# Optimization experiments

Hardware: AMD Instinct MI355X
Metric: run time of the kernel (lower is better)

The kernel has to match this reference:

```python
import jax, jax.numpy as jnp
import numpy as np

R, S, M, K = 512, 48, 4096, 16
RADIUS = 4.0 * 0.025
DIMS = [511, 256, 256, 256, 3]


def posenc(x, n_freqs):
    freqs = 2.0 ** jnp.arange(n_freqs, dtype=x.dtype)
    xf = x[..., None, :] * freqs[:, None]            # [..., F, C]
    sc = jnp.stack([jnp.sin(xf), jnp.cos(xf)], -2)   # [..., F, 2, C]
    return jnp.concatenate([x, sc.reshape(x.shape[:-1] + (-1,))], -1)


def ball_query(q, p, radius, k):
    # pytorch3d-style: first k points (by index order) within radius.
    # dists are squared distances, 0 for padding; neighbors are 0 for padding; idx -1 for padding.
    d2 = jnp.sum((q[:, None, :] - p[None, :, :]) ** 2, -1)    # [Nq, M]
    m = p.shape[0]
    order = jnp.where(d2 < radius * radius, jnp.arange(m), m)
    neg, idx = jax.lax.top_k(-order, k)                        # k smallest valid indices
    valid = neg > -m
    dists = jnp.where(valid, jnp.take_along_axis(d2, idx, axis=1), 0.0)
    nbrs = jnp.where(valid[..., None], p[idx], 0.0)
    return dists, jnp.where(valid, idx, -1), nbrs


def setup_inputs() -> dict:
    key = jax.random.key(0)
    ks = jax.random.split(key, 16)
    inp = {
        "points": jax.random.uniform(ks[0], (R, S, 3), jnp.float32),
        "normals": jax.random.normal(ks[1], (R * S, 3), jnp.float32),
        "view_dirs": jax.random.normal(ks[2], (R * S, 3), jnp.float32),
        "feature_vectors": jax.random.normal(ks[3], (R * S, 256), jnp.float32),
        "indices": 0,
        "physical_particles": jax.random.uniform(ks[4], (M, 3), jnp.float32),
        "rays": jax.random.normal(ks[5], (R, 6), jnp.float32),
        "ro": jax.random.normal(ks[6], (1, 3), jnp.float32),
    }
    for l in range(4):
        scale = (2.0 / DIMS[l + 1]) ** 0.5
        inp[f"W{l}"] = jax.random.normal(ks[7 + l], (DIMS[l + 1], DIMS[l]), jnp.float32) * scale
        inp[f"b{l}"] = jnp.zeros((DIMS[l + 1],), jnp.float32)
    return inp


def reference(points, normals, view_dirs, feature_vectors, indices, physical_particles,
              rays, ro, W0, b0, W1, b1, W2, b2, W3, b3):
    q = points.reshape(-1, 3)                                     # [R*S, 3]
    dists, idx, nbrs = ball_query(q, physical_particles, RADIUS, K)
    dists = dists.reshape(R, S, K)
    nbrs = nbrs.reshape(R, S, K, 3)
    nn_mask = dists != 0                                          # padded entries have dist 0
    num_nn = nn_mask.sum(-1, keepdims=True)                       # [R, S, 1]

    hit_pos_emb = posenc(q, 10)                                   # [R*S, 63]
    hit_dir_emb = jnp.repeat(posenc(rays[:, 3:], 4), S, axis=0)   # [R*S, 27]

    # smoothing_position (exclude_ray=True)
    dn = jnp.linalg.norm(nbrs - points[:, :, None, :], axis=-1)   # [R, S, K]
    w = jnp.maximum(1.0 - (dn / RADIUS) ** 3, 0.0)
    density = w.sum(-1, keepdims=True)                            # [R, S, 1]
    smoothed = (w[..., None] * nbrs).sum(-2) / (density + 1e-12)  # [R, S, 3]

    sp = smoothed.reshape(-1, 3)
    dirs = sp - ro
    dirs = dirs / jnp.linalg.norm(dirs, axis=-1, keepdims=True)

    density_emb = posenc(density.reshape(-1, 1), 4)               # [R*S, 9]
    smoothed_pos_emb = posenc(sp, 10)                             # [R*S, 63]

    # masked variance of neighbor offsets
    diff = jnp.where(nn_mask[..., None], nbrs - points[:, :, None, :], 0.0)
    mean = diff.sum(-2) / (num_nn + 1e-12)
    var = jnp.where(nn_mask[..., None], (diff - mean[:, :, None, :]) ** 2, 0.0).sum(-2) / (num_nn + 1e-12)
    var_emb = posenc(var.reshape(-1, 3), 10)                      # [R*S, 63]

    x = jnp.concatenate([hit_pos_emb, density_emb, smoothed_pos_emb, var_emb,
                         hit_dir_emb, posenc(dirs, 4), normals, feature_vectors], -1)  # [R*S, 511]

    for Wl, bl in ((W0, b0), (W1, b1), (W2, b2)):
        x = jax.nn.relu(x @ Wl.T + bl)
    return jax.nn.sigmoid(x @ W3.T + b3)
```

## Files before the change

### kernel.cpp

```cpp
#include <hip/hip_runtime.h>

typedef _Float16 f16;
typedef f16 f16x8 __attribute__((ext_vector_type(8)));
typedef float f32x4 __attribute__((ext_vector_type(4)));
typedef unsigned short u16;

__device__ __forceinline__ void glds16(const void* g, void* l) {
  __builtin_amdgcn_global_load_lds(
      (const __attribute__((address_space(1))) unsigned*)g,
      (__attribute__((address_space(3))) unsigned*)l, 16, 0, 0);
}


struct FT {
  u16 v[256];
  static constexpr u16 enc(int s, int f, int k) {
    return (u16)(s | (f << 5) | (k << 9));
  }
  constexpr void p3(int base, int F, int src) {
    v[base + 0] = enc(src + 0, 0, 0);
    v[base + 1] = enc(src + 1, 0, 0);
    v[base + 2] = enc(src + 2, 0, 0);
    for (int f = 0; f < F; ++f)
      for (int r = 0; r < 6; ++r) {
        int comp = (r < 3) ? r : r - 3;
        v[base + 3 + f * 6 + r] = enc(src + comp, f, (r < 3) ? 1 : 2);
      }
  }
  constexpr void p1(int base, int F, int src) {
    v[base] = enc(src, 0, 0);
    for (int f = 0; f < F; ++f) {
      v[base + 1 + 2 * f] = enc(src, f, 1);
      v[base + 2 + 2 * f] = enc(src, f, 2);
    }
  }
  constexpr FT() : v{} {
    p3(0, 10, 0);
    p1(63, 4, 3);
    p3(72, 10, 4);
    p3(135, 10, 7);
    p3(198, 4, 10);
    p3(225, 4, 13);
    v[252] = enc(16, 0, 0);
    v[253] = enc(17, 0, 0);
    v[254] = enc(18, 0, 0);
    v[255] = enc(0, 0, 3);
  }
};
__constant__ FT ftab = FT();

__device__ float4 g_sorted[4096];
__device__ int    g_cellStart[1001];

__global__ __launch_bounds__(1024) void setup_kernel(
    const float* __restrict__ parts,
    const float* __restrict__ W0, const float* __restrict__ W1,
    const float* __restrict__ W2,
    f16* __restrict__ w0f, f16* __restrict__ w1f, f16* __restrict__ w2f)
{
  const int tid = threadIdx.x;
  if (blockIdx.x < 256) {
    int i = blockIdx.x * 1024 + tid;
    float v; f16* pf; int n, c;
    if (i < 131072) {
      n = i >> 9; c = i & 511;
      v = (c < 255) ? W0[n * 511 + c] : ((c == 255) ? 0.0f : W0[n * 511 + (c - 1)]);
      pf = w0f;
    } else if (i < 196608) {
      int j = i - 131072; n = j >> 8; c = j & 255; v = W1[j]; pf = w1f;
    } else {
      int j = i - 196608; n = j >> 8; c = j & 255; v = W2[j]; pf = w2f;
    }
    int kt = c >> 5, g = (c >> 3) & 3, jj = c & 7;
    int u = n * 4 + (g ^ ((n >> 1) & 3));
    pf[kt * 8192 + u * 8 + jj] = (f16)v;
  } else {
    __shared__ int cnt[1000];
    __shared__ int pos[1000];
    __shared__ int wpre[125];
    for (int j = tid; j < 1000; j += 1024) cnt[j] = 0;
    __syncthreads();

    float px[4], py[4], pz[4];
    int cd[4];
    #pragma unroll
    for (int t = 0; t < 4; ++t) {
      int i = tid + t * 1024;
      float x = parts[3 * i], y = parts[3 * i + 1], z = parts[3 * i + 2];
      int cx = min(max((int)(x * 10.0f), 0), 9);
      int cy = min(max((int)(y * 10.0f), 0), 9);
      int cz = min(max((int)(z * 10.0f), 0), 9);
      cd[t] = (cz * 10 + cy) * 10 + cx;
      px[t] = x; py[t] = y; pz[t] = z;
      atomicAdd(&cnt[cd[t]], 1);
    }
    __syncthreads();

    if (tid < 125) {
      int s = 0;
      #pragma unroll
      for (int k = 0; k < 8; ++k) s += cnt[tid * 8 + k];
      wpre[tid] = s;
    }
    __syncthreads();
    if (tid == 0) {
      int s = 0;
      for (int c = 0; c < 125; ++c) { int t = wpre[c]; wpre[c] = s; s += t; }
    }
    __syncthreads();
    if (tid < 125) {
      int run = wpre[tid];
      #pragma unroll
      for (int k = 0; k < 8; ++k) {
        int c = tid * 8 + k;
        int n = cnt[c];
        pos[c] = run;
        g_cellStart[c] = run;
        run += n;
      }
    }
    if (tid == 0) g_cellStart[1000] = 4096;
    __syncthreads();

    #pragma unroll
    for (int t = 0; t < 4; ++t) {
      int p = atomicAdd(&pos[cd[t]], 1);
      g_sorted[p] = make_float4(px[t], py[t], pz[t], __int_as_float(tid + t * 1024));
    }
  }
}

#define MAXCH 5

__global__ __launch_bounds__(256) void feat_kernel(
    const float* __restrict__ points, const float* __restrict__ normals,
    const float* __restrict__ parts, const float* __restrict__ rays,
    const float* __restrict__ ro, f16* __restrict__ Xf)
{
  __shared__ float sdata[4][20];

  const int tid = threadIdx.x;
  const int lane = tid & 63, wv = tid >> 6;
  const int q = blockIdx.x * 4 + wv;
  const float qx = points[3 * q], qy = points[3 * q + 1], qz = points[3 * q + 2];
  const float RQ = 0.1f * 0.1f;

  int nAcc = 0;
  float sdx = 0, sdy = 0, sdz = 0;
  float s2x = 0, s2y = 0, s2z = 0;
  float sw = 0, swx = 0, swy = 0, swz = 0;

  const int cqx = min(max((int)(qx * 10.0f), 0), 9);
  const int cqy = min(max((int)(qy * 10.0f), 0), 9);
  const int cqz = min(max((int)(qz * 10.0f), 0), 9);

  int st_l = 0, cn_l = 0;
  if (lane < 9) {
    int dz = lane / 3, dy = lane - dz * 3;
    int cz = cqz - 1 + dz, cy = cqy - 1 + dy;
    if ((unsigned)cz <= 9u && (unsigned)cy <= 9u) {
      int x0 = max(cqx - 1, 0), x1 = min(cqx + 1, 9);
      int rb = (cz * 10 + cy) * 10;
      st_l = g_cellStart[rb + x0];
      cn_l = g_cellStart[rb + x1 + 1] - st_l;
    }
  }

  int pk[9], bk[9];
  int run = 0;
  #pragma unroll
  for (int k = 0; k < 9; ++k) {
    int stk = __builtin_amdgcn_readlane(st_l, k);
    int cnk = __builtin_amdgcn_readlane(cn_l, k);
    pk[k] = run;
    bk[k] = stk - run;
    run += cnk;
  }
  const int C = run;
  const bool fb = (C > MAXCH * 64);

  if (!fb) {
    float4 sv[MAXCH];
    int iv[MAXCH];
    unsigned long long hm[MAXCH];
    #pragma unroll
    for (int ch = 0; ch < MAXCH; ++ch) {
      if (ch * 64 < C) {
        int s = ch * 64 + lane;
        int g = bk[0];
        #pragma unroll
        for (int k = 1; k < 9; ++k) g = (s >= pk[k]) ? bk[k] : g;
        float4 pt = g_sorted[min(g + s, 4095)];
        if (s >= C) {
          pt.x = 1e9f; pt.y = 1e9f; pt.z = 1e9f;
          pt.w = __int_as_float(0x7fffffff);
        }
        sv[ch] = pt;
        iv[ch] = __float_as_int(pt.w);
        float ex = pt.x - qx, ey = pt.y - qy, ez = pt.z - qz;
        float d2 = __fadd_rn(__fadd_rn(__fmul_rn(ex, ex), __fmul_rn(ey, ey)),
                             __fmul_rn(ez, ez));
        hm[ch] = __ballot(d2 < RQ);
      } else {
        hm[ch] = 0ULL;
      }
    }

    int N = 0;
    #pragma unroll
    for (int ch = 0; ch < MAXCH; ++ch) N += __popcll(hm[ch]);

    int thr = 0x7fffffff;
    if (N > 16) {
      int lo = 0, hi = 4095;
      while (lo < hi) {
        int mid = (lo + hi) >> 1;
        int c = 0;
        #pragma unroll
        for (int ch = 0; ch < MAXCH; ++ch)
          if (ch * 64 < C)
            c += __popcll(hm[ch] & __ballot(iv[ch] <= mid));
        if (c >= 16) hi = mid; else lo = mid + 1;
      }
      thr = lo;
    }

    #pragma unroll
    for (int ch = 0; ch < MAXCH; ++ch) {
      if (ch * 64 < C) {
        float4 pt = sv[ch];
        float ex = pt.x - qx, ey = pt.y - qy, ez = pt.z - qz;
        float d2 = __fadd_rn(__fadd_rn(__fmul_rn(ex, ex), __fmul_rn(ey, ey)),
                             __fmul_rn(ez, ez));
        if (d2 < RQ && iv[ch] <= thr) {
          nAcc++;
          sdx += ex; sdy += ey; sdz += ez;
          s2x += ex * ex; s2y += ey * ey; s2z += ez * ez;
          float dn = sqrtf(d2);
          float t = dn * 10.0f;
          float w = fmaxf(1.0f - t * t * t, 0.0f);
          sw += w; swx += w * pt.x; swy += w * pt.y; swz += w * pt.z;
        }
      }
    }
  } else {
    int total = 0;
    for (int jr = 0; jr < 64; ++jr) {
      int pi = jr * 64 + lane;
      float x = parts[3 * pi], y = parts[3 * pi + 1], z = parts[3 * pi + 2];
      float ex = x - qx, ey = y - qy, ez = z - qz;
      float d2 = __fadd_rn(__fadd_rn(__fmul_rn(ex, ex), __fmul_rn(ey, ey)),
                           __fmul_rn(ez, ez));
      bool hit = d2 < RQ;
      unsigned long long m = __ballot(hit);
      int pos = __builtin_amdgcn_mbcnt_hi((unsigned)(m >> 32),
                __builtin_amdgcn_mbcnt_lo((unsigned)m, 0u));
      if (hit && (total + pos < 16)) {
        nAcc++;
        sdx += ex; sdy += ey; sdz += ez;
        s2x += ex * ex; s2y += ey * ey; s2z += ez * ez;
        float dn = sqrtf(d2);
        float t = dn * 10.0f;
        float w = fmaxf(1.0f - t * t * t, 0.0f);
        sw += w; swx += w * x; swy += w * y; swz += w * z;
      }
      total += __popcll(m);
      if (total >= 16) break;
    }
  }

  #define WRED(x) { _Pragma("unroll") for (int o = 32; o; o >>= 1) x += __shfl_xor(x, o, 64); }
  float fn = (float)nAcc;
  WRED(fn); WRED(sdx); WRED(sdy); WRED(sdz);
  WRED(s2x); WRED(s2y); WRED(s2z);
  WRED(sw); WRED(swx); WRED(swy); WRED(swz);
  #undef WRED

  float tq = sqrtf(qx * qx + qy * qy + qz * qz) * 10.0f;
  float wpad = fmaxf(1.0f - tq * tq * tq, 0.0f);
  float density = sw + (16.0f - fn) * wpad;
  float invd = 1.0f / (density + 1e-12f);
  float spx = swx * invd, spy = swy * invd, spz = swz * invd;

  float invn = 1.0f / (fn + 1e-12f);
  float mx = sdx * invn, my = sdy * invn, mz = sdz * invn;
  float vx = fmaxf((s2x - 2.0f * mx * sdx + fn * mx * mx) * invn, 0.0f);
  float vy = fmaxf((s2y - 2.0f * my * sdy + fn * my * my) * invn, 0.0f);
  float vz = fmaxf((s2z - 2.0f * mz * sdz + fn * mz * mz) * invn, 0.0f);

  float dxx = spx - ro[0], dyy = spy - ro[1], dzz = spz - ro[2];
  float il = 1.0f / sqrtf(dxx * dxx + dyy * dyy + dzz * dzz);

  if (lane == 0) {
    float* s = sdata[wv];
    s[0] = qx; s[1] = qy; s[2] = qz; s[3] = density;
    s[4] = spx; s[5] = spy; s[6] = spz;
    s[7] = vx; s[8] = vy; s[9] = vz;
    int r = q / 48;
    s[10] = rays[6 * r + 3]; s[11] = rays[6 * r + 4]; s[12] = rays[6 * r + 5];
    s[13] = dxx * il; s[14] = dyy * il; s[15] = dzz * il;
    s[16] = normals[3 * q]; s[17] = normals[3 * q + 1]; s[18] = normals[3 * q + 2];
  }
  __syncthreads();

  const int b = q / 48, m48 = q % 48;
  const size_t base = (size_t)b * 12288;
  #pragma unroll
  for (int it = 0; it < 4; ++it) {
    int c = it * 64 + lane;
    int e = ftab.v[c];
    float sv_ = sdata[wv][e & 31];
    float arg = sv_ * (float)(1 << ((e >> 5) & 15));
    float sn, cs;
    __sincosf(arg, &sn, &cs);
    int kind = e >> 9;
    float val = (kind == 0) ? sv_ : (kind == 1 ? sn : (kind == 2 ? cs : 0.0f));
    int kt = c >> 5, g = (c >> 3) & 3, j = c & 7;
    int u = m48 * 4 + (g ^ ((m48 >> 1) & 3));
    Xf[base + kt * 1536 + u * 8 + j] = (f16)val;
  }
}

__global__ __launch_bounds__(512, 6) void fused_mlp(
    const f16* __restrict__ Xf, const float* __restrict__ fvec,
    const f16* __restrict__ w0f, const f16* __restrict__ w1f,
    const f16* __restrict__ w2f,
    const float* __restrict__ b0, const float* __restrict__ b1,
    const float* __restrict__ b2,
    const float* __restrict__ W3, const float* __restrict__ b3,
    float* __restrict__ out)
{
  extern __shared__ char lds[];
  f16* As = (f16*)lds;
  f16* Hf = (f16*)lds;
  f16* H2 = (f16*)(lds + 24576);
  float* w3s = (float*)(lds + 49152);

  const int tid = threadIdx.x, lane = tid & 63, wn = tid >> 6;
  const int l15 = lane & 15, l4 = lane >> 4;
  const int blk = blockIdx.x;

  f32x4 acc[3][2];
  f16x8 bq[4][2];
  f16x8 af[2][3];

  const f16* Xft = Xf + (size_t)blk * 12288;

  int uB[2];
  #pragma unroll
  for (int j = 0; j < 2; ++j) {
    int n = wn * 32 + j * 16 + l15;
    uB[j] = n * 4 + (l4 ^ ((n >> 1) & 3));
  }
  int uA[3];
  #pragma unroll
  for (int i = 0; i < 3; ++i) {
    int m = i * 16 + l15;
    uA[i] = m * 4 + (l4 ^ ((m >> 1) & 3));
  }

  auto zacc = [&]() {
    #pragma unroll
    for (int i = 0; i < 3; ++i)
      #pragma unroll
      for (int j = 0; j < 2; ++j) acc[i][j] = (f32x4){0, 0, 0, 0};
  };
  auto loadB = [&](const f16* wf, int kt, f16x8* bf) {
    #pragma unroll
    for (int j = 0; j < 2; ++j)
      bf[j] = *(const f16x8*)(wf + kt * 8192 + uB[j] * 8);
  };
  auto loadA0 = [&](int kt, f16x8* a3) {
    #pragma unroll
    for (int i = 0; i < 3; ++i)
      a3[i] = *(const f16x8*)(As + kt * 1536 + uA[i] * 8);
  };
  auto loadAH = [&](const f16* Hsrc, int kt, f16x8* a3) {
    #pragma unroll
    for (int i = 0; i < 3; ++i) {
      int m = i * 16 + l15;
      int g = kt * 4 + l4;
      int u = m * 32 + (g ^ ((m >> 1) & 7));
      a3[i] = *(const f16x8*)(Hsrc + u * 8);
    }
  };
  auto mfmas = [&](f16x8* a3, f16x8* b2) {
    #pragma unroll
    for (int i = 0; i < 3; ++i)
      #pragma unroll
      for (int j = 0; j < 2; ++j)
        acc[i][j] = __builtin_amdgcn_mfma_f32_16x16x32_f16(a3[i], b2[j], acc[i][j], 0, 0, 0);
  };
  auto epilogue = [&](const float* bias_, f16* Hdst) {
    float bv[2];
    #pragma unroll
    for (int j = 0; j < 2; ++j) bv[j] = bias_[wn * 32 + j * 16 + l15];
    #pragma unroll
    for (int i = 0; i < 3; ++i) {
      #pragma unroll
      for (int r = 0; r < 4; ++r) {
        int m = i * 16 + l4 * 4 + r;
        #pragma unroll
        for (int j = 0; j < 2; ++j) {
          int n = wn * 32 + j * 16 + l15;
          float v = fmaxf(acc[i][j][r] + bv[j], 0.0f);
          int u = m * 32 + ((n >> 3) ^ ((m >> 1) & 7));
          Hdst[u * 8 + (n & 7)] = (f16)v;
        }
      }
    }
  };

  #pragma unroll
  for (int r = 0; r < 3; ++r)
    glds16(Xft + r * 4096 + tid * 8, As + r * 4096 + tid * 8);
  if (tid < 384) {
    int m = tid >> 3, sub = tid & 7, g = sub & 3, kh = sub >> 2;
    int u = m * 4 + (g ^ ((m >> 1) & 3));
    #pragma unroll
    for (int t = 0; t < 4; ++t) {
      int kf = kh * 4 + t;
      const float* src = fvec + (size_t)(blk * 48 + m) * 256 + kf * 32 + g * 8;
      float4 v0 = ((const float4*)src)[0];
      float4 v1 = ((const float4*)src)[1];
      f16 hs[8] = {(f16)v0.x, (f16)v0.y, (f16)v0.z, (f16)v0.w,
                   (f16)v1.x, (f16)v1.y, (f16)v1.z, (f16)v1.w};
      *(uint4*)(As + (8 + kf) * 1536 + u * 8) = *(uint4*)hs;
    }
  }
  loadB(w0f, 0, bq[0]);
  loadB(w0f, 1, bq[1]);
  loadB(w0f, 2, bq[2]);
  __syncthreads();

  zacc();
  loadA0(0, af[0]);
  #pragma unroll
  for (int kt = 0; kt < 16; ++kt) {
    if (kt < 13) loadB(w0f, kt + 3, bq[(kt + 3) & 3]);
    if (kt < 15) loadA0(kt + 1, af[(kt + 1) & 1]);
    mfmas(af[kt & 1], bq[kt & 3]);
  }
  loadB(w1f, 0, bq[0]);
  loadB(w1f, 1, bq[1]);
  loadB(w1f, 2, bq[2]);
  __syncthreads();
  epilogue(b0, Hf);
  __syncthreads();

  zacc();
  loadAH(Hf, 0, af[0]);
  #pragma unroll
  for (int kt = 0; kt < 8; ++kt) {
    if (kt < 5) loadB(w1f, kt + 3, bq[(kt + 3) & 3]);
    if (kt < 7) loadAH(Hf, kt + 1, af[(kt + 1) & 1]);
    mfmas(af[kt & 1], bq[kt & 3]);
  }
  loadB(w2f, 0, bq[0]);
  loadB(w2f, 1, bq[1]);
  loadB(w2f, 2, bq[2]);
  epilogue(b1, H2);
  __syncthreads();

  zacc();
  loadAH(H2, 0, af[0]);
  #pragma unroll
  for (int kt = 0; kt < 8; ++kt) {
    if (kt < 5) loadB(w2f, kt + 3, bq[(kt + 3) & 3]);
    if (kt < 7) loadAH(H2, kt + 1, af[(kt + 1) & 1]);
    mfmas(af[kt & 1], bq[kt & 3]);
  }
  epilogue(b2, Hf);
  __syncthreads();

  for (int i = tid; i < 768; i += 512) w3s[i] = W3[i];
  __syncthreads();

  const float B30 = b3[0], B31 = b3[1], B32 = b3[2];
  #pragma unroll 1
  for (int rr = 0; rr < 6; ++rr) {
    int m = wn * 6 + rr;
    int g = lane >> 1, j0 = (lane & 1) * 4;
    int u = m * 32 + (g ^ ((m >> 1) & 7));
    uint2 pk = *(const uint2*)(Hf + u * 8 + j0);
    f16 h4[4];
    *(uint2*)h4 = pk;
    float h0 = (float)h4[0], h1 = (float)h4[1], h2 = (float)h4[2], h3 = (float)h4[3];
    int kc = lane * 4;
    float4 wa = *(const float4*)(w3s + kc);
    float4 wb = *(const float4*)(w3s + 256 + kc);
    float4 wc = *(const float4*)(w3s + 512 + kc);
    float p0 = fmaf(h3, wa.w, fmaf(h2, wa.z, fmaf(h1, wa.y, h0 * wa.x)));
    float p1 = fmaf(h3, wb.w, fmaf(h2, wb.z, fmaf(h1, wb.y, h0 * wb.x)));
    float p2 = fmaf(h3, wc.w, fmaf(h2, wc.z, fmaf(h1, wc.y, h0 * wc.x)));
    #pragma unroll
    for (int o = 32; o; o >>= 1) {
      p0 += __shfl_xor(p0, o, 64);
      p1 += __shfl_xor(p1, o, 64);
      p2 += __shfl_xor(p2, o, 64);
    }
    if (lane == 0) {
      size_t ro_ = (size_t)(blk * 48 + m) * 3;
      out[ro_ + 0] = 1.0f / (1.0f + expf(-(p0 + B30)));
      out[ro_ + 1] = 1.0f / (1.0f + expf(-(p1 + B31)));
      out[ro_ + 2] = 1.0f / (1.0f + expf(-(p2 + B32)));
    }
  }
}

extern "C" void kernel_launch(void* const* d_in, const int* in_sizes, int n_in,
                              void* d_out, int out_size, void* d_ws, size_t ws_size,
                              hipStream_t stream) {
  const float* points  = (const float*)d_in[0];
  const float* normals = (const float*)d_in[1];
  const float* fvec    = (const float*)d_in[3];
  const float* parts   = (const float*)d_in[5];
  const float* rays    = (const float*)d_in[6];
  const float* ro      = (const float*)d_in[7];
  const float* W0 = (const float*)d_in[8];
  const float* b0 = (const float*)d_in[9];
  const float* W1 = (const float*)d_in[10];
  const float* b1 = (const float*)d_in[11];
  const float* W2 = (const float*)d_in[12];
  const float* b2 = (const float*)d_in[13];
  const float* W3 = (const float*)d_in[14];
  const float* b3 = (const float*)d_in[15];

  char* ws = (char*)d_ws;
  f16* Xf  = (f16*)(ws);
  f16* w0f = (f16*)(ws + 12582912);
  f16* w1f = (f16*)(ws + 12845056);
  f16* w2f = (f16*)(ws + 12976128);
  float* out = (float*)d_out;

  (void)hipFuncSetAttribute((const void*)fused_mlp,
                            hipFuncAttributeMaxDynamicSharedMemorySize, 52224);

  setup_kernel<<<257, 1024, 0, stream>>>(parts, W0, W1, W2, w0f, w1f, w2f);
  feat_kernel<<<6144, 256, 0, stream>>>(points, normals, parts, rays, ro, Xf);
  fused_mlp<<<512, 512, 52224, stream>>>(Xf, fvec, w0f, w1f, w2f,
                                         b0, b1, b2, W3, b3, out);
}
```

Measured before the change: 159.9 us.

## Fuse feature-embedding kernel into MLP kernel, building inputs directly in LDS

Merges the ball-query/feature kernel into the fused MLP kernel. Each 512-thread block now computes the neighbor statistics and positional encodings for its 48 samples, one wave per six queries, and writes the f16 input tile straight into shared memory. This removes the 12 MB global Xf round trip and one kernel launch. In exchange, the ball-query work runs serially inside the MLP blocks with fewer concurrent waves, which may lengthen the kernel's critical path.

```diff
diff --git a/kernel.cpp b/kernel.cpp
--- a/kernel.cpp
+++ b/kernel.cpp
@@ -4,12 +4,6 @@
 typedef f16 f16x8 __attribute__((ext_vector_type(8)));
 typedef float f32x4 __attribute__((ext_vector_type(4)));
 typedef unsigned short u16;
-
-__device__ __forceinline__ void glds16(const void* g, void* l) {
-  __builtin_amdgcn_global_load_lds(
-      (const __attribute__((address_space(1))) unsigned*)g,
-      (__attribute__((address_space(3))) unsigned*)l, 16, 0, 0);
-}
 
 
 struct FT {
@@ -132,197 +126,10 @@
 
 #define MAXCH 5
 
-__global__ __launch_bounds__(256) void feat_kernel(
+__global__ __launch_bounds__(512, 6) void fused_all(
     const float* __restrict__ points, const float* __restrict__ normals,
-    const float* __restrict__ parts, const float* __restrict__ rays,
-    const float* __restrict__ ro, f16* __restrict__ Xf)
-{
-  __shared__ float sdata[4][20];
-
-  const int tid = threadIdx.x;
-  const int lane = tid & 63, wv = tid >> 6;
-  const int q = blockIdx.x * 4 + wv;
-  const float qx = points[3 * q], qy = points[3 * q + 1], qz = points[3 * q + 2];
-  const float RQ = 0.1f * 0.1f;
-
-  int nAcc = 0;
-  float sdx = 0, sdy = 0, sdz = 0;
-  float s2x = 0, s2y = 0, s2z = 0;
-  float sw = 0, swx = 0, swy = 0, swz = 0;
-
-  const int cqx = min(max((int)(qx * 10.0f), 0), 9);
-  const int cqy = min(max((int)(qy * 10.0f), 0), 9);
-  const int cqz = min(max((int)(qz * 10.0f), 0), 9);
-
-  int st_l = 0, cn_l = 0;
-  if (lane < 9) {
-    int dz = lane / 3, dy = lane - dz * 3;
-    int cz = cqz - 1 + dz, cy = cqy - 1 + dy;
-    if ((unsigned)cz <= 9u && (unsigned)cy <= 9u) {
-      int x0 = max(cqx - 1, 0), x1 = min(cqx + 1, 9);
-      int rb = (cz * 10 + cy) * 10;
-      st_l = g_cellStart[rb + x0];
-      cn_l = g_cellStart[rb + x1 + 1] - st_l;
-    }
-  }
-
-  int pk[9], bk[9];
-  int run = 0;
-  #pragma unroll
-  for (int k = 0; k < 9; ++k) {
-    int stk = __builtin_amdgcn_readlane(st_l, k);
-    int cnk = __builtin_amdgcn_readlane(cn_l, k);
-    pk[k] = run;
-    bk[k] = stk - run;
-    run += cnk;
-  }
-  const int C = run;
-  const bool fb = (C > MAXCH * 64);
-
-  if (!fb) {
-    float4 sv[MAXCH];
-    int iv[MAXCH];
-    unsigned long long hm[MAXCH];
-    #pragma unroll
-    for (int ch = 0; ch < MAXCH; ++ch) {
-      if (ch * 64 < C) {
-        int s = ch * 64 + lane;
-        int g = bk[0];
-        #pragma unroll
-        for (int k = 1; k < 9; ++k) g = (s >= pk[k]) ? bk[k] : g;
-        float4 pt = g_sorted[min(g + s, 4095)];
-        if (s >= C) {
-          pt.x = 1e9f; pt.y = 1e9f; pt.z = 1e9f;
-          pt.w = __int_as_float(0x7fffffff);
-        }
-        sv[ch] = pt;
-        iv[ch] = __float_as_int(pt.w);
-        float ex = pt.x - qx, ey = pt.y - qy, ez = pt.z - qz;
-        float d2 = __fadd_rn(__fadd_rn(__fmul_rn(ex, ex), __fmul_rn(ey, ey)),
-                             __fmul_rn(ez, ez));
-        hm[ch] = __ballot(d2 < RQ);
-      } else {
-        hm[ch] = 0ULL;
-      }
-    }
-
-    int N = 0;
-    #pragma unroll
-    for (int ch = 0; ch < MAXCH; ++ch) N += __popcll(hm[ch]);
-
-    int thr = 0x7fffffff;
-    if (N > 16) {
-      int lo = 0, hi = 4095;
-      while (lo < hi) {
-        int mid = (lo + hi) >> 1;
-        int c = 0;
-        #pragma unroll
-        for (int ch = 0; ch < MAXCH; ++ch)
-          if (ch * 64 < C)
-            c += __popcll(hm[ch] & __ballot(iv[ch] <= mid));
-        if (c >= 16) hi = mid; else lo = mid + 1;
-      }
-      thr = lo;
-    }
-
-    #pragma unroll
-    for (int ch = 0; ch < MAXCH; ++ch) {
-      if (ch * 64 < C) {
-        float4 pt = sv[ch];
-        float ex = pt.x - qx, ey = pt.y - qy, ez = pt.z - qz;
-        float d2 = __fadd_rn(__fadd_rn(__fmul_rn(ex, ex), __fmul_rn(ey, ey)),
-                             __fmul_rn(ez, ez));
-        if (d2 < RQ && iv[ch] <= thr) {
-          nAcc++;
-          sdx += ex; sdy += ey; sdz += ez;
-          s2x += ex * ex; s2y += ey * ey; s2z += ez * ez;
-          float dn = sqrtf(d2);
-          float t = dn * 10.0f;
-          float w = fmaxf(1.0f - t * t * t, 0.0f);
-          sw += w; swx += w * pt.x; swy += w * pt.y; swz += w * pt.z;
-        }
-      }
-    }
-  } else {
-    int total = 0;
-    for (int jr = 0; jr < 64; ++jr) {
-      int pi = jr * 64 + lane;
-      float x = parts[3 * pi], y = parts[3 * pi + 1], z = parts[3 * pi + 2];
-      float ex = x - qx, ey = y - qy, ez = z - qz;
-      float d2 = __fadd_rn(__fadd_rn(__fmul_rn(ex, ex), __fmul_rn(ey, ey)),
-                           __fmul_rn(ez, ez));
-      bool hit = d2 < RQ;
-      unsigned long long m = __ballot(hit);
-      int pos = __builtin_amdgcn_mbcnt_hi((unsigned)(m >> 32),
-                __builtin_amdgcn_mbcnt_lo((unsigned)m, 0u));
-      if (hit && (total + pos < 16)) {
-        nAcc++;
-        sdx += ex; sdy += ey; sdz += ez;
-        s2x += ex * ex; s2y += ey * ey; s2z += ez * ez;
-        float dn = sqrtf(d2);
-        float t = dn * 10.0f;
-        float w = fmaxf(1.0f - t * t * t, 0.0f);
-        sw += w; swx += w * x; swy += w * y; swz += w * z;
-      }
-      total += __popcll(m);
-      if (total >= 16) break;
-    }
-  }
-
-  #define WRED(x) { _Pragma("unroll") for (int o = 32; o; o >>= 1) x += __shfl_xor(x, o, 64); }
-  float fn = (float)nAcc;
-  WRED(fn); WRED(sdx); WRED(sdy); WRED(sdz);
-  WRED(s2x); WRED(s2y); WRED(s2z);
-  WRED(sw); WRED(swx); WRED(swy); WRED(swz);
-  #undef WRED
-
-  float tq = sqrtf(qx * qx + qy * qy + qz * qz) * 10.0f;
-  float wpad = fmaxf(1.0f - tq * tq * tq, 0.0f);
-  float density = sw + (16.0f - fn) * wpad;
-  float invd = 1.0f / (density + 1e-12f);
-  float spx = swx * invd, spy = swy * invd, spz = swz * invd;
-
-  float invn = 1.0f / (fn + 1e-12f);
-  float mx = sdx * invn, my = sdy * invn, mz = sdz * invn;
-  float vx = fmaxf((s2x - 2.0f * mx * sdx + fn * mx * mx) * invn, 0.0f);
-  float vy = fmaxf((s2y - 2.0f * my * sdy + fn * my * my) * invn, 0.0f);
-  float vz = fmaxf((s2z - 2.0f * mz * sdz + fn * mz * mz) * invn, 0.0f);
-
-  float dxx = spx - ro[0], dyy = spy - ro[1], dzz = spz - ro[2];
-  float il = 1.0f / sqrtf(dxx * dxx + dyy * dyy + dzz * dzz);
-
-  if (lane == 0) {
-    float* s = sdata[wv];
-    s[0] = qx; s[1] = qy; s[2] = qz; s[3] = density;
-    s[4] = spx; s[5] = spy; s[6] = spz;
-    s[7] = vx; s[8] = vy; s[9] = vz;
-    int r = q / 48;
-    s[10] = rays[6 * r + 3]; s[11] = rays[6 * r + 4]; s[12] = rays[6 * r + 5];
-    s[13] = dxx * il; s[14] = dyy * il; s[15] = dzz * il;
-    s[16] = normals[3 * q]; s[17] = normals[3 * q + 1]; s[18] = normals[3 * q + 2];
-  }
-  __syncthreads();
-
-  const int b = q / 48, m48 = q % 48;
-  const size_t base = (size_t)b * 12288;
-  #pragma unroll
-  for (int it = 0; it < 4; ++it) {
-    int c = it * 64 + lane;
-    int e = ftab.v[c];
-    float sv_ = sdata[wv][e & 31];
-    float arg = sv_ * (float)(1 << ((e >> 5) & 15));
-    float sn, cs;
-    __sincosf(arg, &sn, &cs);
-    int kind = e >> 9;
-    float val = (kind == 0) ? sv_ : (kind == 1 ? sn : (kind == 2 ? cs : 0.0f));
-    int kt = c >> 5, g = (c >> 3) & 3, j = c & 7;
-    int u = m48 * 4 + (g ^ ((m48 >> 1) & 3));
-    Xf[base + kt * 1536 + u * 8 + j] = (f16)val;
-  }
-}
-
-__global__ __launch_bounds__(512, 6) void fused_mlp(
-    const f16* __restrict__ Xf, const float* __restrict__ fvec,
+    const float* __restrict__ fvec, const float* __restrict__ rays,
+    const float* __restrict__ ro, const float* __restrict__ parts,
     const f16* __restrict__ w0f, const f16* __restrict__ w1f,
     const f16* __restrict__ w2f,
     const float* __restrict__ b0, const float* __restrict__ b1,
@@ -334,17 +141,216 @@
   f16* As = (f16*)lds;
   f16* Hf = (f16*)lds;
   f16* H2 = (f16*)(lds + 24576);
+  float* sdata = (float*)(lds + 49152);
   float* w3s = (float*)(lds + 49152);
 
   const int tid = threadIdx.x, lane = tid & 63, wn = tid >> 6;
   const int l15 = lane & 15, l4 = lane >> 4;
   const int blk = blockIdx.x;
 
+  if (tid < 384) {
+    int m = tid >> 3, sub = tid & 7, g = sub & 3, kh = sub >> 2;
+    int u = m * 4 + (g ^ ((m >> 1) & 3));
+    #pragma unroll
+    for (int t = 0; t < 4; ++t) {
+      int kf = kh * 4 + t;
+      const float* src = fvec + (size_t)(blk * 48 + m) * 256 + kf * 32 + g * 8;
+      float4 v0 = ((const float4*)src)[0];
+      float4 v1 = ((const float4*)src)[1];
+      f16 hs[8] = {(f16)v0.x, (f16)v0.y, (f16)v0.z, (f16)v0.w,
+                   (f16)v1.x, (f16)v1.y, (f16)v1.z, (f16)v1.w};
+      *(uint4*)(As + (8 + kf) * 1536 + u * 8) = *(uint4*)hs;
+    }
+  }
+
+  const float RQ = 0.1f * 0.1f;
+  #pragma unroll 1
+  for (int t = 0; t < 6; ++t) {
+    const int m48 = wn * 6 + t;
+    const int q = blk * 48 + m48;
+    const float qx = points[3 * q], qy = points[3 * q + 1], qz = points[3 * q + 2];
+
+    int nAcc = 0;
+    float sdx = 0, sdy = 0, sdz = 0;
+    float s2x = 0, s2y = 0, s2z = 0;
+    float sw = 0, swx = 0, swy = 0, swz = 0;
+
+    const int cqx = min(max((int)(qx * 10.0f), 0), 9);
+    const int cqy = min(max((int)(qy * 10.0f), 0), 9);
+    const int cqz = min(max((int)(qz * 10.0f), 0), 9);
+
+    int st_l = 0, cn_l = 0;
+    if (lane < 9) {
+      int dz = lane / 3, dy = lane - dz * 3;
+      int cz = cqz - 1 + dz, cy = cqy - 1 + dy;
+      if ((unsigned)cz <= 9u && (unsigned)cy <= 9u) {
+        int x0 = max(cqx - 1, 0), x1 = min(cqx + 1, 9);
+        int rb = (cz * 10 + cy) * 10;
+        st_l = g_cellStart[rb + x0];
+        cn_l = g_cellStart[rb + x1 + 1] - st_l;
+      }
+    }
+
+    int pk[9], bk[9];
+    int run = 0;
+    #pragma unroll
+    for (int k = 0; k < 9; ++k) {
+      int stk = __builtin_amdgcn_readlane(st_l, k);
+      int cnk = __builtin_amdgcn_readlane(cn_l, k);
+      pk[k] = run;
+      bk[k] = stk - run;
+      run += cnk;
+    }
+    const int C = run;
+    const bool fb = (C > MAXCH * 64);
+
+    if (!fb) {
+      float4 sv[MAXCH];
+      int iv[MAXCH];
+      unsigned long long hm[MAXCH];
+      #pragma unroll
+      for (int ch = 0; ch < MAXCH; ++ch) {
+        if (ch * 64 < C) {
+          int s = ch * 64 + lane;
+          int g = bk[0];
+          #pragma unroll
+          for (int k = 1; k < 9; ++k) g = (s >= pk[k]) ? bk[k] : g;
+          float4 pt = g_sorted[min(g + s, 4095)];
+          if (s >= C) {
+            pt.x = 1e9f; pt.y = 1e9f; pt.z = 1e9f;
+            pt.w = __int_as_float(0x7fffffff);
+          }
+          sv[ch] = pt;
+          iv[ch] = __float_as_int(pt.w);
+          float ex = pt.x - qx, ey = pt.y - qy, ez = pt.z - qz;
+          float d2 = __fadd_rn(__fadd_rn(__fmul_rn(ex, ex), __fmul_rn(ey, ey)),
+                               __fmul_rn(ez, ez));
+          hm[ch] = __ballot(d2 < RQ);
+        } else {
+          hm[ch] = 0ULL;
+        }
+      }
+
+      int N = 0;
+      #pragma unroll
+      for (int ch = 0; ch < MAXCH; ++ch) N += __popcll(hm[ch]);
+
+      int thr = 0x7fffffff;
+      if (N > 16) {
+        int lo = 0, hi = 4095;
+        while (lo < hi) {
+          int mid = (lo + hi) >> 1;
+          int c = 0;
+          #pragma unroll
+          for (int ch = 0; ch < MAXCH; ++ch)
+            if (ch * 64 < C)
+              c += __popcll(hm[ch] & __ballot(iv[ch] <= mid));
+          if (c >= 16) hi = mid; else lo = mid + 1;
+        }
+        thr = lo;
+      }
+
+      #pragma unroll
+      for (int ch = 0; ch < MAXCH; ++ch) {
+        if (ch * 64 < C) {
+          float4 pt = sv[ch];
+          float ex = pt.x - qx, ey = pt.y - qy, ez = pt.z - qz;
+          float d2 = __fadd_rn(__fadd_rn(__fmul_rn(ex, ex), __fmul_rn(ey, ey)),
+                               __fmul_rn(ez, ez));
+          if (d2 < RQ && iv[ch] <= thr) {
+            nAcc++;
+            sdx += ex; sdy += ey; sdz += ez;
+            s2x += ex * ex; s2y += ey * ey; s2z += ez * ez;
+            float dn = sqrtf(d2);
+            float tt = dn * 10.0f;
+            float w = fmaxf(1.0f - tt * tt * tt, 0.0f);
+            sw += w; swx += w * pt.x; swy += w * pt.y; swz += w * pt.z;
+          }
+        }
+      }
+    } else {
+      int total = 0;
+      for (int jr = 0; jr < 64; ++jr) {
+        int pi = jr * 64 + lane;
+        float x = parts[3 * pi], y = parts[3 * pi + 1], z = parts[3 * pi + 2];
+        float ex = x - qx, ey = y - qy, ez = z - qz;
+        float d2 = __fadd_rn(__fadd_rn(__fmul_rn(ex, ex), __fmul_rn(ey, ey)),
+                             __fmul_rn(ez, ez));
+        bool hit = d2 < RQ;
+        unsigned long long m = __ballot(hit);
+        int pos = __builtin_amdgcn_mbcnt_hi((unsigned)(m >> 32),
+                  __builtin_amdgcn_mbcnt_lo((unsigned)m, 0u));
+        if (hit && (total + pos < 16)) {
+          nAcc++;
+          sdx += ex; sdy += ey; sdz += ez;
+          s2x += ex * ex; s2y += ey * ey; s2z += ez * ez;
+          float dn = sqrtf(d2);
+          float tt = dn * 10.0f;
+          float w = fmaxf(1.0f - tt * tt * tt, 0.0f);
+          sw += w; swx += w * x; swy += w * y; swz += w * z;
+        }
+        total += __popcll(m);
+        if (total >= 16) break;
+      }
+    }
+
+    #define WRED(x) { _Pragma("unroll") for (int o = 32; o; o >>= 1) x += __shfl_xor(x, o, 64); }
+    float fn = (float)nAcc;
+    WRED(fn); WRED(sdx); WRED(sdy); WRED(sdz);
+    WRED(s2x); WRED(s2y); WRED(s2z);
+    WRED(sw); WRED(swx); WRED(swy); WRED(swz);
+    #undef WRED
+
+    float tq = sqrtf(qx * qx + qy * qy + qz * qz) * 10.0f;
+    float wpad = fmaxf(1.0f - tq * tq * tq, 0.0f);
+    float density = sw + (16.0f - fn) * wpad;
+    float invd = 1.0f / (density + 1e-12f);
+    float spx = swx * invd, spy = swy * invd, spz = swz * invd;
+
+    float invn = 1.0f / (fn + 1e-12f);
+    float mx = sdx * invn, my = sdy * invn, mz = sdz * invn;
+    float vx = fmaxf((s2x - 2.0f * mx * sdx + fn * mx * mx) * invn, 0.0f);
+    float vy = fmaxf((s2y - 2.0f * my * sdy + fn * my * my) * invn, 0.0f);
+    float vz = fmaxf((s2z - 2.0f * mz * sdz + fn * mz * mz) * invn, 0.0f);
+
+    float dxx = spx - ro[0], dyy = spy - ro[1], dzz = spz - ro[2];
+    float il = 1.0f / sqrtf(dxx * dxx + dyy * dyy + dzz * dzz);
+
+    if (lane == 0) {
+      float* s = sdata + m48 * 20;
+      s[0] = qx; s[1] = qy; s[2] = qz; s[3] = density;
+      s[4] = spx; s[5] = spy; s[6] = spz;
+      s[7] = vx; s[8] = vy; s[9] = vz;
+      s[10] = rays[6 * blk + 3]; s[11] = rays[6 * blk + 4]; s[12] = rays[6 * blk + 5];
+      s[13] = dxx * il; s[14] = dyy * il; s[15] = dzz * il;
+      s[16] = normals[3 * q]; s[17] = normals[3 * q + 1]; s[18] = normals[3 * q + 2];
+    }
+  }
+  __syncthreads();
+
+  #pragma unroll 1
+  for (int t = 0; t < 6; ++t) {
+    const int m48 = wn * 6 + t;
+    const float* s = sdata + m48 * 20;
+    #pragma unroll
+    for (int it = 0; it < 4; ++it) {
+      int c = it * 64 + lane;
+      int e = ftab.v[c];
+      float sv_ = s[e & 31];
+      float arg = sv_ * (float)(1 << ((e >> 5) & 15));
+      float sn, cs;
+      __sincosf(arg, &sn, &cs);
+      int kind = e >> 9;
+      float val = (kind == 0) ? sv_ : (kind == 1 ? sn : (kind == 2 ? cs : 0.0f));
+      int kt = c >> 5, g = (c >> 3) & 3, j = c & 7;
+      int u = m48 * 4 + (g ^ ((m48 >> 1) & 3));
+      As[kt * 1536 + u * 8 + j] = (f16)val;
+    }
+  }
+
   f32x4 acc[3][2];
   f16x8 bq[4][2];
   f16x8 af[2][3];
-
-  const f16* Xft = Xf + (size_t)blk * 12288;
 
   int uB[2];
   #pragma unroll
@@ -411,23 +417,6 @@
     }
   };
 
-  #pragma unroll
-  for (int r = 0; r < 3; ++r)
-    glds16(Xft + r * 4096 + tid * 8, As + r * 4096 + tid * 8);
-  if (tid < 384) {
-    int m = tid >> 3, sub = tid & 7, g = sub & 3, kh = sub >> 2;
-    int u = m * 4 + (g ^ ((m >> 1) & 3));
-    #pragma unroll
-    for (int t = 0; t < 4; ++t) {
-      int kf = kh * 4 + t;
-      const float* src = fvec + (size_t)(blk * 48 + m) * 256 + kf * 32 + g * 8;
-      float4 v0 = ((const float4*)src)[0];
-      float4 v1 = ((const float4*)src)[1];
-      f16 hs[8] = {(f16)v0.x, (f16)v0.y, (f16)v0.z, (f16)v0.w,
-                   (f16)v1.x, (f16)v1.y, (f16)v1.z, (f16)v1.w};
-      *(uint4*)(As + (8 + kf) * 1536 + u * 8) = *(uint4*)hs;
-    }
-  }
   loadB(w0f, 0, bq[0]);
   loadB(w0f, 1, bq[1]);
   loadB(w0f, 2, bq[2]);
@@ -527,17 +516,16 @@
   const float* b3 = (const float*)d_in[15];
 
   char* ws = (char*)d_ws;
-  f16* Xf  = (f16*)(ws);
-  f16* w0f = (f16*)(ws + 12582912);
-  f16* w1f = (f16*)(ws + 12845056);
-  f16* w2f = (f16*)(ws + 12976128);
+  f16* w0f = (f16*)(ws);
+  f16* w1f = (f16*)(ws + 262144);
+  f16* w2f = (f16*)(ws + 393216);
   float* out = (float*)d_out;
 
-  (void)hipFuncSetAttribute((const void*)fused_mlp,
-                            hipFuncAttributeMaxDynamicSharedMemorySize, 52224);
+  (void)hipFuncSetAttribute((const void*)fused_all,
+                            hipFuncAttributeMaxDynamicSharedMemorySize, 52992);
 
   setup_kernel<<<257, 1024, 0, stream>>>(parts, W0, W1, W2, w0f, w1f, w2f);
-  feat_kernel<<<6144, 256, 0, stream>>>(points, normals, parts, rays, ro, Xf);
-  fused_mlp<<<512, 512, 52224, stream>>>(Xf, fvec, w0f, w1f, w2f,
+  fused_all<<<512, 512, 52992, stream>>>(points, normals, fvec, rays, ro, parts,
+                                         w0f, w1f, w2f,
                                          b0, b1, b2, W3, b3, out);
 }
```

Result: slower. 167.5 us (+4.7%).
